# Kernel optimization log

Hardware: AMD Instinct MI355X
Metric: run time of the kernel (lower is better)

The kernel has to match this reference:

```python
import jax, jax.numpy as jnp
import numpy as np
import math

CLASSES = 1024
IN_F = 32
OUT_F = 32
N = 262144


def setup_inputs() -> dict:
    key = jax.random.key(0)
    k1, k2, k3, k4 = jax.random.split(key, 4)
    k = math.sqrt(1.0 / float(IN_F))
    inp = jax.random.normal(k1, (N, IN_F), dtype=jnp.float32)
    inds = jax.random.randint(k2, (N,), 0, CLASSES, dtype=jnp.int32)
    w = jax.random.uniform(k3, (CLASSES, IN_F, OUT_F), dtype=jnp.float32, minval=-k, maxval=k)
    b = jax.random.uniform(k4, (CLASSES, 1, OUT_F), dtype=jnp.float32, minval=-k, maxval=k)
    return {"input": inp, "inds": inds, "w": w, "b": b}


def reference(input, inds, w, b):
    # per-row expert matmul: out[n] = input[n] @ w[inds[n]] + b[inds[n]]
    w_g = w[inds]            # [n, in, out] gathered expert weights
    b_g = b[inds, 0]         # [n, out]
    return jnp.einsum('ni,nio->no', input, w_g) + b_g
```

## Files before the change

### kernel.cpp

```cpp
#include <hip/hip_runtime.h>


#define N_ROWS      262144
#define N_CLASSES   1024
#define IN_F        32
#define OUT_F       32
#define HIST_BLOCKS 64
#define ROWS_PER_HB (N_ROWS / HIST_BLOCKS)

__global__ __launch_bounds__(256) void k_hist(const int* __restrict__ inds,
                                              int* __restrict__ bc) {
    __shared__ int h[N_CLASSES];
    const int tid = threadIdx.x;
    for (int c = tid; c < N_CLASSES; c += 256) h[c] = 0;
    __syncthreads();
    const int base = blockIdx.x * ROWS_PER_HB;
    for (int k = 0; k < ROWS_PER_HB; k += 256) {
        int c = inds[base + k + tid];
        atomicAdd(&h[c], 1);
    }
    __syncthreads();
    for (int c = tid; c < N_CLASSES; c += 256)
        bc[blockIdx.x * N_CLASSES + c] = h[c];
}

__global__ __launch_bounds__(1024) void k_scan(int* __restrict__ bc,
                                               int* __restrict__ cls_off) {
    __shared__ int s[N_CLASSES];
    const int c = threadIdx.x;
    int total = 0;
    for (int b = 0; b < HIST_BLOCKS; ++b) total += bc[b * N_CLASSES + c];
    s[c] = total;
    __syncthreads();
    for (int off = 1; off < N_CLASSES; off <<= 1) {
        int v = (c >= off) ? s[c - off] : 0;
        __syncthreads();
        s[c] += v;
        __syncthreads();
    }
    const int base = s[c] - total;
    cls_off[c] = base;
    if (c == N_CLASSES - 1) cls_off[N_CLASSES] = s[c];
    int run = base;
    for (int b = 0; b < HIST_BLOCKS; ++b) {
        int t = bc[b * N_CLASSES + c];
        bc[b * N_CLASSES + c] = run;
        run += t;
    }
}

__global__ __launch_bounds__(256) void k_scatter(const int* __restrict__ inds,
                                                 const int* __restrict__ bc,
                                                 int* __restrict__ rowids) {
    __shared__ int cur[N_CLASSES];
    const int tid = threadIdx.x;
    for (int c = tid; c < N_CLASSES; c += 256)
        cur[c] = bc[blockIdx.x * N_CLASSES + c];
    __syncthreads();
    const int base = blockIdx.x * ROWS_PER_HB;
    for (int k = 0; k < ROWS_PER_HB; k += 256) {
        int row = base + k + tid;
        int c = inds[row];
        int pos = atomicAdd(&cur[c], 1);
        rowids[pos] = row;
    }
}

__global__ __launch_bounds__(256) void k_condmul(const float* __restrict__ input,
                                                 const float* __restrict__ w,
                                                 const float* __restrict__ bias,
                                                 const int* __restrict__ rowids,
                                                 const int* __restrict__ cls_off,
                                                 float* __restrict__ out) {
    __shared__ float wlds[IN_F * OUT_F];
    const int cls = blockIdx.x;
    const int tid = threadIdx.x;

    ((float4*)wlds)[tid] = ((const float4*)(w + (size_t)cls * IN_F * OUT_F))[tid];

    const int oq = tid & 7;
    const int rg = tid >> 3;
    const float4 bv = ((const float4*)(bias + (size_t)cls * OUT_F))[oq];
    const int start = cls_off[cls];
    const int count = cls_off[cls + 1] - start;
    __syncthreads();

    const float4* wl4 = (const float4*)wlds;
    const int iters = (count + 31) >> 5;
    for (int it = 0; it < iters; ++it) {
        const int ri = it * 32 + rg;
        const bool valid = ri < count;
        const int idx = valid ? ri : (count - 1);
        const int row = rowids[start + idx];

        const float4* xin = (const float4*)(input + (size_t)row * IN_F);
        float4 x[8];
#pragma unroll
        for (int j = 0; j < 8; ++j) x[j] = xin[j];

        float4 acc = bv;
#pragma unroll
        for (int j = 0; j < 8; ++j) {
            const float a0 = x[j].x, a1 = x[j].y, a2 = x[j].z, a3 = x[j].w;
            const float4 w0 = wl4[(j * 4 + 0) * (OUT_F / 4) + oq];
            const float4 w1 = wl4[(j * 4 + 1) * (OUT_F / 4) + oq];
            const float4 w2 = wl4[(j * 4 + 2) * (OUT_F / 4) + oq];
            const float4 w3 = wl4[(j * 4 + 3) * (OUT_F / 4) + oq];
            acc.x += a0 * w0.x; acc.y += a0 * w0.y; acc.z += a0 * w0.z; acc.w += a0 * w0.w;
            acc.x += a1 * w1.x; acc.y += a1 * w1.y; acc.z += a1 * w1.z; acc.w += a1 * w1.w;
            acc.x += a2 * w2.x; acc.y += a2 * w2.y; acc.z += a2 * w2.z; acc.w += a2 * w2.w;
            acc.x += a3 * w3.x; acc.y += a3 * w3.y; acc.z += a3 * w3.z; acc.w += a3 * w3.w;
        }
        if (valid)
            ((float4*)(out + (size_t)row * OUT_F))[oq] = acc;
    }
}

__global__ __launch_bounds__(256) void k_naive(const float* __restrict__ input,
                                               const int* __restrict__ inds,
                                               const float* __restrict__ w,
                                               const float* __restrict__ bias,
                                               float* __restrict__ out) {
    const int tid = threadIdx.x;
    const int oq = tid & 7;
    const int rg = tid >> 3;
    const int row = blockIdx.x * 32 + rg;
    if (row >= N_ROWS) return;
    const int c = inds[row];
    const float4* xin = (const float4*)(input + (size_t)row * IN_F);
    const float4* wr = (const float4*)(w + (size_t)c * IN_F * OUT_F);
    float4 acc = ((const float4*)(bias + (size_t)c * OUT_F))[oq];
#pragma unroll
    for (int j = 0; j < 8; ++j) {
        const float4 xv = xin[j];
        const float a0 = xv.x, a1 = xv.y, a2 = xv.z, a3 = xv.w;
        const float4 w0 = wr[(j * 4 + 0) * (OUT_F / 4) + oq];
        const float4 w1 = wr[(j * 4 + 1) * (OUT_F / 4) + oq];
        const float4 w2 = wr[(j * 4 + 2) * (OUT_F / 4) + oq];
        const float4 w3 = wr[(j * 4 + 3) * (OUT_F / 4) + oq];
        acc.x += a0 * w0.x; acc.y += a0 * w0.y; acc.z += a0 * w0.z; acc.w += a0 * w0.w;
        acc.x += a1 * w1.x; acc.y += a1 * w1.y; acc.z += a1 * w1.z; acc.w += a1 * w1.w;
        acc.x += a2 * w2.x; acc.y += a2 * w2.y; acc.z += a2 * w2.z; acc.w += a2 * w2.w;
        acc.x += a3 * w3.x; acc.y += a3 * w3.y; acc.z += a3 * w3.z; acc.w += a3 * w3.w;
    }
    ((float4*)(out + (size_t)row * OUT_F))[oq] = acc;
}

extern "C" void kernel_launch(void* const* d_in, const int* in_sizes, int n_in,
                              void* d_out, int out_size, void* d_ws, size_t ws_size,
                              hipStream_t stream) {
    const float* input = (const float*)d_in[0];
    const int*   inds  = (const int*)d_in[1];
    const float* w     = (const float*)d_in[2];
    const float* bias  = (const float*)d_in[3];
    float* out = (float*)d_out;

    int* ws = (int*)d_ws;
    int* bc      = ws;
    int* cls_off = ws + HIST_BLOCKS * N_CLASSES;
    int* rowids  = cls_off + N_CLASSES + 1 + 3;
    const size_t need = (size_t)(HIST_BLOCKS * N_CLASSES + N_CLASSES + 4 + N_ROWS) * sizeof(int);

    if (ws_size >= need) {
        k_hist<<<HIST_BLOCKS, 256, 0, stream>>>(inds, bc);
        k_scan<<<1, 1024, 0, stream>>>(bc, cls_off);
        k_scatter<<<HIST_BLOCKS, 256, 0, stream>>>(inds, bc, rowids);
        k_condmul<<<N_CLASSES, 256, 0, stream>>>(input, w, bias, rowids, cls_off, out);
    } else {
        k_naive<<<N_ROWS / 32, 256, 0, stream>>>(input, inds, w, bias, out);
    }
}
```

Before: 121.7 us.

## Use global atomic cursors for scatter, keep weights in registers, two rows per thread

The scan kernel now writes only per-class base offsets into a global cursor array, replacing the serial per-block prefix pass. The scatter kernel then claims positions with global atomics instead of LDS cursors, and both histogram and scatter use twice as many blocks. The matmul kernel holds each thread's weight column slice in registers rather than LDS, processes two rows per iteration for more memory parallelism, and skips empty classes. Global atomics on 1024 counters may contend, the row order within a class becomes nondeterministic, and the register-resident weights raise register pressure.

```diff
diff --git a/kernel.cpp b/kernel.cpp
--- a/kernel.cpp
+++ b/kernel.cpp
@@ -5,8 +5,8 @@
 #define N_CLASSES   1024
 #define IN_F        32
 #define OUT_F       32
-#define HIST_BLOCKS 64
-#define ROWS_PER_HB (N_ROWS / HIST_BLOCKS)
+#define HB          128
+#define ROWS_PER_HB (N_ROWS / HB)
 
 __global__ __launch_bounds__(256) void k_hist(const int* __restrict__ inds,
                                               int* __restrict__ bc) {
@@ -15,21 +15,21 @@
     for (int c = tid; c < N_CLASSES; c += 256) h[c] = 0;
     __syncthreads();
     const int base = blockIdx.x * ROWS_PER_HB;
-    for (int k = 0; k < ROWS_PER_HB; k += 256) {
-        int c = inds[base + k + tid];
-        atomicAdd(&h[c], 1);
-    }
+    for (int k = 0; k < ROWS_PER_HB; k += 256)
+        atomicAdd(&h[inds[base + k + tid]], 1);
     __syncthreads();
     for (int c = tid; c < N_CLASSES; c += 256)
         bc[blockIdx.x * N_CLASSES + c] = h[c];
 }
 
-__global__ __launch_bounds__(1024) void k_scan(int* __restrict__ bc,
-                                               int* __restrict__ cls_off) {
+__global__ __launch_bounds__(1024) void k_scan(const int* __restrict__ bc,
+                                               int* __restrict__ cls_off,
+                                               int* __restrict__ cursor) {
     __shared__ int s[N_CLASSES];
     const int c = threadIdx.x;
     int total = 0;
-    for (int b = 0; b < HIST_BLOCKS; ++b) total += bc[b * N_CLASSES + c];
+#pragma unroll 8
+    for (int b = 0; b < HB; ++b) total += bc[b * N_CLASSES + c];
     s[c] = total;
     __syncthreads();
     for (int off = 1; off < N_CLASSES; off <<= 1) {
@@ -40,79 +40,83 @@
     }
     const int base = s[c] - total;
     cls_off[c] = base;
+    cursor[c]  = base;
     if (c == N_CLASSES - 1) cls_off[N_CLASSES] = s[c];
-    int run = base;
-    for (int b = 0; b < HIST_BLOCKS; ++b) {
-        int t = bc[b * N_CLASSES + c];
-        bc[b * N_CLASSES + c] = run;
-        run += t;
-    }
 }
 
 __global__ __launch_bounds__(256) void k_scatter(const int* __restrict__ inds,
-                                                 const int* __restrict__ bc,
+                                                 int* __restrict__ cursor,
                                                  int* __restrict__ rowids) {
-    __shared__ int cur[N_CLASSES];
+    const int base = blockIdx.x * ROWS_PER_HB;
     const int tid = threadIdx.x;
-    for (int c = tid; c < N_CLASSES; c += 256)
-        cur[c] = bc[blockIdx.x * N_CLASSES + c];
-    __syncthreads();
-    const int base = blockIdx.x * ROWS_PER_HB;
     for (int k = 0; k < ROWS_PER_HB; k += 256) {
-        int row = base + k + tid;
-        int c = inds[row];
-        int pos = atomicAdd(&cur[c], 1);
+        const int row = base + k + tid;
+        const int c = inds[row];
+        const int pos = atomicAdd(&cursor[c], 1);
         rowids[pos] = row;
     }
 }
 
-__global__ __launch_bounds__(256) void k_condmul(const float* __restrict__ input,
-                                                 const float* __restrict__ w,
-                                                 const float* __restrict__ bias,
-                                                 const int* __restrict__ rowids,
-                                                 const int* __restrict__ cls_off,
-                                                 float* __restrict__ out) {
-    __shared__ float wlds[IN_F * OUT_F];
+__global__ __launch_bounds__(256, 2) void k_condmul(const float* __restrict__ input,
+                                                    const float* __restrict__ w,
+                                                    const float* __restrict__ bias,
+                                                    const int* __restrict__ rowids,
+                                                    const int* __restrict__ cls_off,
+                                                    float* __restrict__ out) {
     const int cls = blockIdx.x;
     const int tid = threadIdx.x;
-
-    ((float4*)wlds)[tid] = ((const float4*)(w + (size_t)cls * IN_F * OUT_F))[tid];
-
     const int oq = tid & 7;
     const int rg = tid >> 3;
-    const float4 bv = ((const float4*)(bias + (size_t)cls * OUT_F))[oq];
+
     const int start = cls_off[cls];
     const int count = cls_off[cls + 1] - start;
-    __syncthreads();
+    if (count <= 0) return;
 
-    const float4* wl4 = (const float4*)wlds;
-    const int iters = (count + 31) >> 5;
+    const float4* w4 = (const float4*)(w + (size_t)cls * (IN_F * OUT_F));
+    float4 wr[IN_F];
+#pragma unroll
+    for (int j = 0; j < IN_F; ++j) wr[j] = w4[j * (OUT_F / 4) + oq];
+
+    const float4 bv = ((const float4*)(bias + (size_t)cls * OUT_F))[oq];
+
+    const int iters = (count + 63) >> 6;
     for (int it = 0; it < iters; ++it) {
-        const int ri = it * 32 + rg;
-        const bool valid = ri < count;
-        const int idx = valid ? ri : (count - 1);
-        const int row = rowids[start + idx];
+        const int riA = it * 64 + rg;
+        const int riB = riA + 32;
+        const bool va = riA < count;
+        const bool vb = riB < count;
+        const int rowA = rowids[start + (va ? riA : count - 1)];
+        const int rowB = rowids[start + (vb ? riB : count - 1)];
 
-        const float4* xin = (const float4*)(input + (size_t)row * IN_F);
-        float4 x[8];
+        const float4* xa4 = (const float4*)(input + (size_t)rowA * IN_F);
+        const float4* xb4 = (const float4*)(input + (size_t)rowB * IN_F);
+        float4 xa[8], xb[8];
 #pragma unroll
-        for (int j = 0; j < 8; ++j) x[j] = xin[j];
+        for (int j = 0; j < 8; ++j) xa[j] = xa4[j];
+#pragma unroll
+        for (int j = 0; j < 8; ++j) xb[j] = xb4[j];
 
-        float4 acc = bv;
+        float4 accA = bv;
+        float4 accB = bv;
 #pragma unroll
         for (int j = 0; j < 8; ++j) {
-            const float a0 = x[j].x, a1 = x[j].y, a2 = x[j].z, a3 = x[j].w;
-            const float4 w0 = wl4[(j * 4 + 0) * (OUT_F / 4) + oq];
-            const float4 w1 = wl4[(j * 4 + 1) * (OUT_F / 4) + oq];
-            const float4 w2 = wl4[(j * 4 + 2) * (OUT_F / 4) + oq];
-            const float4 w3 = wl4[(j * 4 + 3) * (OUT_F / 4) + oq];
-            acc.x += a0 * w0.x; acc.y += a0 * w0.y; acc.z += a0 * w0.z; acc.w += a0 * w0.w;
-            acc.x += a1 * w1.x; acc.y += a1 * w1.y; acc.z += a1 * w1.z; acc.w += a1 * w1.w;
-            acc.x += a2 * w2.x; acc.y += a2 * w2.y; acc.z += a2 * w2.z; acc.w += a2 * w2.w;
-            acc.x += a3 * w3.x; acc.y += a3 * w3.y; acc.z += a3 * w3.z; acc.w += a3 * w3.w;
+            const float a0 = xa[j].x, a1 = xa[j].y, a2 = xa[j].z, a3 = xa[j].w;
+            const float b0 = xb[j].x, b1 = xb[j].y, b2 = xb[j].z, b3 = xb[j].w;
+            const float4 w0 = wr[j * 4 + 0];
+            const float4 w1 = wr[j * 4 + 1];
+            const float4 w2 = wr[j * 4 + 2];
+            const float4 w3 = wr[j * 4 + 3];
+            accA.x += a0 * w0.x; accA.y += a0 * w0.y; accA.z += a0 * w0.z; accA.w += a0 * w0.w;
+            accA.x += a1 * w1.x; accA.y += a1 * w1.y; accA.z += a1 * w1.z; accA.w += a1 * w1.w;
+            accA.x += a2 * w2.x; accA.y += a2 * w2.y; accA.z += a2 * w2.z; accA.w += a2 * w2.w;
+            accA.x += a3 * w3.x; accA.y += a3 * w3.y; accA.z += a3 * w3.z; accA.w += a3 * w3.w;
+            accB.x += b0 * w0.x; accB.y += b0 * w0.y; accB.z += b0 * w0.z; accB.w += b0 * w0.w;
+            accB.x += b1 * w1.x; accB.y += b1 * w1.y; accB.z += b1 * w1.z; accB.w += b1 * w1.w;
+            accB.x += b2 * w2.x; accB.y += b2 * w2.y; accB.z += b2 * w2.z; accB.w += b2 * w2.w;
+            accB.x += b3 * w3.x; accB.y += b3 * w3.y; accB.z += b3 * w3.z; accB.w += b3 * w3.w;
         }
-        if (valid)
-            ((float4*)(out + (size_t)row * OUT_F))[oq] = acc;
+        if (va) ((float4*)(out + (size_t)rowA * OUT_F))[oq] = accA;
+        if (vb) ((float4*)(out + (size_t)rowB * OUT_F))[oq] = accB;
     }
 }
 
@@ -157,14 +161,15 @@
 
     int* ws = (int*)d_ws;
     int* bc      = ws;
-    int* cls_off = ws + HIST_BLOCKS * N_CLASSES;
-    int* rowids  = cls_off + N_CLASSES + 1 + 3;
-    const size_t need = (size_t)(HIST_BLOCKS * N_CLASSES + N_CLASSES + 4 + N_ROWS) * sizeof(int);
+    int* cls_off = ws + HB * N_CLASSES;
+    int* cursor  = cls_off + N_CLASSES + 1 + 3;
+    int* rowids  = cursor + N_CLASSES;
+    const size_t need = (size_t)(HB * N_CLASSES + N_CLASSES + 4 + N_CLASSES + N_ROWS) * sizeof(int);
 
     if (ws_size >= need) {
-        k_hist<<<HIST_BLOCKS, 256, 0, stream>>>(inds, bc);
-        k_scan<<<1, 1024, 0, stream>>>(bc, cls_off);
-        k_scatter<<<HIST_BLOCKS, 256, 0, stream>>>(inds, bc, rowids);
+        k_hist<<<HB, 256, 0, stream>>>(inds, bc);
+        k_scan<<<1, 1024, 0, stream>>>(bc, cls_off, cursor);
+        k_scatter<<<HB, 256, 0, stream>>>(inds, cursor, rowids);
         k_condmul<<<N_CLASSES, 256, 0, stream>>>(input, w, bias, rowids, cls_off, out);
     } else {
         k_naive<<<N_ROWS / 32, 256, 0, stream>>>(input, inds, w, bias, out);
```

Measured after the change: 179.6 us. 47.5% more time.

## Transpose block-count matrix and split per-block offset pass into separate kernel

Applied to the files above, without the earlier changes.

Stores the per-block class histogram transposed (class-major) so the single-block scan reads each class's 64 counts as contiguous int4 loads. The per-block running-offset computation moves out of the one-block scan kernel into a new 4-block kernel that does vectorized read-modify-write. This removes serial strided global traffic from the single 1024-thread block. The cost is an extra kernel launch, and the histogram writes and scatter reads become strided.

```diff
diff --git a/kernel.cpp b/kernel.cpp
--- a/kernel.cpp
+++ b/kernel.cpp
@@ -5,31 +5,34 @@
 #define N_CLASSES   1024
 #define IN_F        32
 #define OUT_F       32
-#define HIST_BLOCKS 64
-#define ROWS_PER_HB (N_ROWS / HIST_BLOCKS)
+#define HB          64
+#define ROWS_PER_HB (N_ROWS / HB)
 
 __global__ __launch_bounds__(256) void k_hist(const int* __restrict__ inds,
-                                              int* __restrict__ bc) {
+                                              int* __restrict__ bcT) {
     __shared__ int h[N_CLASSES];
     const int tid = threadIdx.x;
     for (int c = tid; c < N_CLASSES; c += 256) h[c] = 0;
     __syncthreads();
     const int base = blockIdx.x * ROWS_PER_HB;
-    for (int k = 0; k < ROWS_PER_HB; k += 256) {
-        int c = inds[base + k + tid];
-        atomicAdd(&h[c], 1);
-    }
+    for (int k = 0; k < ROWS_PER_HB; k += 256)
+        atomicAdd(&h[inds[base + k + tid]], 1);
     __syncthreads();
     for (int c = tid; c < N_CLASSES; c += 256)
-        bc[blockIdx.x * N_CLASSES + c] = h[c];
+        bcT[c * HB + blockIdx.x] = h[c];
 }
 
-__global__ __launch_bounds__(1024) void k_scan(int* __restrict__ bc,
+__global__ __launch_bounds__(1024) void k_scan(const int* __restrict__ bcT,
                                                int* __restrict__ cls_off) {
     __shared__ int s[N_CLASSES];
     const int c = threadIdx.x;
+    const int4* p = (const int4*)(bcT + c * HB);
     int total = 0;
-    for (int b = 0; b < HIST_BLOCKS; ++b) total += bc[b * N_CLASSES + c];
+#pragma unroll
+    for (int j = 0; j < HB / 4; ++j) {
+        const int4 t = p[j];
+        total += t.x + t.y + t.z + t.w;
+    }
     s[c] = total;
     __syncthreads();
     for (int off = 1; off < N_CLASSES; off <<= 1) {
@@ -38,30 +41,40 @@
         s[c] += v;
         __syncthreads();
     }
-    const int base = s[c] - total;
-    cls_off[c] = base;
+    cls_off[c] = s[c] - total;
     if (c == N_CLASSES - 1) cls_off[N_CLASSES] = s[c];
-    int run = base;
-    for (int b = 0; b < HIST_BLOCKS; ++b) {
-        int t = bc[b * N_CLASSES + c];
-        bc[b * N_CLASSES + c] = run;
-        run += t;
+}
+
+__global__ __launch_bounds__(256) void k_offsets(int* __restrict__ bcT,
+                                                 const int* __restrict__ cls_off) {
+    const int c = blockIdx.x * 256 + threadIdx.x;
+    int run = cls_off[c];
+    int4* p = (int4*)(bcT + c * HB);
+#pragma unroll
+    for (int j = 0; j < HB / 4; ++j) {
+        const int4 t = p[j];
+        int4 o;
+        o.x = run; run += t.x;
+        o.y = run; run += t.y;
+        o.z = run; run += t.z;
+        o.w = run; run += t.w;
+        p[j] = o;
     }
 }
 
 __global__ __launch_bounds__(256) void k_scatter(const int* __restrict__ inds,
-                                                 const int* __restrict__ bc,
+                                                 const int* __restrict__ bcT,
                                                  int* __restrict__ rowids) {
     __shared__ int cur[N_CLASSES];
     const int tid = threadIdx.x;
     for (int c = tid; c < N_CLASSES; c += 256)
-        cur[c] = bc[blockIdx.x * N_CLASSES + c];
+        cur[c] = bcT[c * HB + blockIdx.x];
     __syncthreads();
     const int base = blockIdx.x * ROWS_PER_HB;
     for (int k = 0; k < ROWS_PER_HB; k += 256) {
-        int row = base + k + tid;
-        int c = inds[row];
-        int pos = atomicAdd(&cur[c], 1);
+        const int row = base + k + tid;
+        const int c = inds[row];
+        const int pos = atomicAdd(&cur[c], 1);
         rowids[pos] = row;
     }
 }
@@ -156,15 +169,16 @@
     float* out = (float*)d_out;
 
     int* ws = (int*)d_ws;
-    int* bc      = ws;
-    int* cls_off = ws + HIST_BLOCKS * N_CLASSES;
+    int* bcT     = ws;
+    int* cls_off = ws + N_CLASSES * HB;
     int* rowids  = cls_off + N_CLASSES + 1 + 3;
-    const size_t need = (size_t)(HIST_BLOCKS * N_CLASSES + N_CLASSES + 4 + N_ROWS) * sizeof(int);
+    const size_t need = (size_t)(N_CLASSES * HB + N_CLASSES + 4 + N_ROWS) * sizeof(int);
 
     if (ws_size >= need) {
-        k_hist<<<HIST_BLOCKS, 256, 0, stream>>>(inds, bc);
-        k_scan<<<1, 1024, 0, stream>>>(bc, cls_off);
-        k_scatter<<<HIST_BLOCKS, 256, 0, stream>>>(inds, bc, rowids);
+        k_hist<<<HB, 256, 0, stream>>>(inds, bcT);
+        k_scan<<<1, 1024, 0, stream>>>(bcT, cls_off);
+        k_offsets<<<N_CLASSES / 256, 256, 0, stream>>>(bcT, cls_off);
+        k_scatter<<<HB, 256, 0, stream>>>(inds, bcT, rowids);
         k_condmul<<<N_CLASSES, 256, 0, stream>>>(input, w, bias, rowids, cls_off, out);
     } else {
         k_naive<<<N_ROWS / 32, 256, 0, stream>>>(input, inds, w, bias, out);
```

Result: slower. 125.2 us (+2.8%).
